# Optimization experiments

Measured on AMD Instinct MI355X. Metric: run time of the kernel, lower is better.

Reference implementation:

```python
import jax, jax.numpy as jnp
import numpy as np

EMBEDDING_DIM = 512
HEAD_DIM = 64
B, T_NEW, T_CACHE = 8, 1024, 3072
T_TOTAL = T_NEW + T_CACHE


def setup_inputs() -> dict:
    key = jax.random.key(0)
    ks = jax.random.split(key, 6)
    x = jax.random.normal(ks[0], (B, T_NEW, EMBEDDING_DIM), dtype=jnp.float32)
    cache_k = jax.random.normal(ks[1], (B, T_CACHE, HEAD_DIM), dtype=jnp.float32)
    cache_v = jax.random.normal(ks[2], (B, T_CACHE, HEAD_DIM), dtype=jnp.float32)
    # Causal mask rows for the new tokens: cache fully visible, causal among new.
    # Equivalent to tril(ones(T_TOTAL, T_TOTAL))[T_CACHE:, :].
    rows = jnp.arange(T_NEW)[:, None] + T_CACHE  # absolute positions of new tokens
    cols = jnp.arange(T_TOTAL)[None, :]
    mask = (cols <= rows).astype(jnp.int32)  # [T_NEW, T_TOTAL]
    scale = 1.0 / np.sqrt(EMBEDDING_DIM)
    Wq = jax.random.normal(ks[3], (EMBEDDING_DIM, HEAD_DIM), dtype=jnp.float32) * scale
    Wk = jax.random.normal(ks[4], (EMBEDDING_DIM, HEAD_DIM), dtype=jnp.float32) * scale
    Wv = jax.random.normal(ks[5], (EMBEDDING_DIM, HEAD_DIM), dtype=jnp.float32) * scale
    return {"x": x, "mask": mask, "cache_k": cache_k, "cache_v": cache_v,
            "Wq": Wq, "Wk": Wk, "Wv": Wv}


def reference(x, mask, cache_k, cache_v, Wq, Wk, Wv):
    # Projections (nn.Linear with bias=False)
    q = jnp.einsum("btc,cd->btd", x, Wq)  # [B, T_new, D]
    k_new = jnp.einsum("btc,cd->btd", x, Wk)
    v_new = jnp.einsum("btc,cd->btd", x, Wv)
    k = jnp.concatenate([cache_k, k_new], axis=1)  # [B, T_total, D]
    v = jnp.concatenate([cache_v, v_new], axis=1)
    d = k.shape[-1]
    scores = jnp.einsum("btd,bsd->bts", q, k) * (d ** -0.5)  # [B, T_new, T_total]
    T = q.shape[1]
    cur_mask = mask[:T, :k.shape[1]]  # [T_new, T_total]
    scores = jnp.where(cur_mask == 0, jnp.float32(-jnp.inf), scores)
    probs = jax.nn.softmax(scores, axis=-1)
    # Dropout is identity in eval mode (deterministic reference).
    out = jnp.einsum("bts,bsd->btd", probs, v)  # [B, T_new, D]
    return out, k, v
```

## Files before the change

kernel.cpp:

```cpp
#include <hip/hip_runtime.h>

#define NB     8
#define TNEW   1024
#define TCACHE 3072
#define TTOT   4096
#define EMB    512
#define HD     64

typedef __bf16 bf16x8 __attribute__((ext_vector_type(8)));
typedef __bf16 bf16x4 __attribute__((ext_vector_type(4)));
typedef float  f32x4  __attribute__((ext_vector_type(4)));

#define MFMA(a,b,c) __builtin_amdgcn_mfma_f32_16x16x32_bf16((a),(b),(c),0,0,0)

#define GLOAD_LDS16(g, l) \
    __builtin_amdgcn_global_load_lds((const __attribute__((address_space(1))) void*)(g), \
                                     (__attribute__((address_space(3))) void*)(l), 16, 0, 0)

#define QSCALE 0.180336880f

#define WS_WT   0
#define WS_KBF  196608
#define WS_VTB  4390912
#define WS_OP   8585216
#define WS_ML   16973824


__global__ __launch_bounds__(256) void prep(const float* __restrict__ ck,
                                            const float* __restrict__ cv,
                                            const float* __restrict__ Wq,
                                            const float* __restrict__ Wk,
                                            const float* __restrict__ Wv,
                                            float* __restrict__ kout,
                                            float* __restrict__ vout,
                                            __bf16* __restrict__ kb,
                                            __bf16* __restrict__ vtb,
                                            __bf16* __restrict__ wt) {
    __shared__ __bf16 vl[64][72];
    const int blk = blockIdx.x;
    const int tid = threadIdx.x;
    if (blk < 768) {
#pragma unroll
        for (int it = 0; it < 2; ++it) {
            const int i = blk * 256 + tid + it * 196608;
            const int b = i / 49152;
            const int f = i - b * 49152;
            const int s = f >> 4, d = (f & 15) * 4;
            const float4 kd = ((const float4*)ck)[i];
            ((float4*)(kout + (size_t)b * TTOT * HD))[f] = kd;
            bf16x4 k4;
            k4[0] = (__bf16)kd.x; k4[1] = (__bf16)kd.y;
            k4[2] = (__bf16)kd.z; k4[3] = (__bf16)kd.w;
            *(bf16x4*)(kb + (size_t)b * TTOT * HD + s * HD + d) = k4;
        }
    } else if (blk < 1152) {
        const int tb = blk - 768;
        const int b = tb / 48, si = tb - (tb / 48) * 48;
        const int sbase = si * 64;
        const float4* src = (const float4*)(cv + ((size_t)b * TCACHE + sbase) * HD);
        float4* dstf = (float4*)(vout + ((size_t)b * TTOT + sbase) * HD);
#pragma unroll
        for (int k = 0; k < 4; ++k) {
            const int f = tid + 256 * k;
            const int s = f >> 4, d4 = (f & 15) * 4;
            const float4 v = src[f];
            dstf[f] = v;
            bf16x4 t;
            t[0] = (__bf16)v.x; t[1] = (__bf16)v.y;
            t[2] = (__bf16)v.z; t[3] = (__bf16)v.w;
            *(bf16x4*)&vl[s][d4] = t;
        }
        __syncthreads();
        const int d = tid >> 2, sc = tid & 3;
        __bf16* vt = vtb + ((size_t)b * HD + d) * TTOT + sbase + (sc >> 1) * 32 + (sc & 1) * 4;
#pragma unroll
        for (int t4 = 0; t4 < 4; ++t4) {
            bf16x4 o;
#pragma unroll
            for (int c = 0; c < 4; ++c) o[c] = vl[sc * 16 + t4 * 4 + c][d];
            *(bf16x4*)(vt + t4 * 8) = o;
        }
    } else {
        const int tb = blk - 1152;
        const int m = tb >> 3;
        const int ct = (tb & 7) * 64;
        const float* W = (m == 0) ? Wq : (m == 1) ? Wk : Wv;
        const float4* src = (const float4*)(W + (size_t)ct * HD);
#pragma unroll
        for (int k = 0; k < 4; ++k) {
            const int f = tid + 256 * k;
            const int c = f >> 4, d4 = (f & 15) * 4;
            const float4 v = src[f];
            bf16x4 t;
            t[0] = (__bf16)v.x; t[1] = (__bf16)v.y;
            t[2] = (__bf16)v.z; t[3] = (__bf16)v.w;
            *(bf16x4*)&vl[c][d4] = t;
        }
        __syncthreads();
        const int d = tid >> 2, sc = tid & 3;
        bf16x8 o0, o1;
#pragma unroll
        for (int i = 0; i < 8; ++i) {
            o0[i] = vl[sc * 16 + i][d];
            o1[i] = vl[sc * 16 + 8 + i][d];
        }
        __bf16* wr = wt + (size_t)m * HD * EMB + (size_t)d * EMB + ct + sc * 16;
        *(bf16x8*)wr = o0;
        *(bf16x8*)(wr + 8) = o1;
    }
}

__global__ __launch_bounds__(128) void proj_mfma(const float* __restrict__ x,
                                                 const __bf16* __restrict__ wt,
                                                 __bf16* __restrict__ qb,
                                                 float* __restrict__ kout,
                                                 float* __restrict__ vout,
                                                 __bf16* __restrict__ kb,
                                                 __bf16* __restrict__ vtb) {
    __shared__ __bf16 xs[32][520];
    __shared__ __bf16 vls[2][64][24];
    const int tid = threadIdx.x;
    const int w = tid >> 6, lane = tid & 63;
    const int lo = lane & 15, hi = lane >> 4;
    const int r0 = blockIdx.x * 32 + w * 16;
    const int b = r0 >> 10;
    const int t0r = r0 & (TNEW - 1);

    {
        const float4* xg = (const float4*)(x + (size_t)blockIdx.x * 32 * EMB);
#pragma unroll
        for (int k = 0; k < 32; ++k) {
            const int f = tid + 128 * k;
            const int row = f >> 7, col4 = (f & 127) * 4;
            const float4 v = xg[f];
            bf16x4 t;
            t[0] = (__bf16)v.x; t[1] = (__bf16)v.y;
            t[2] = (__bf16)v.z; t[3] = (__bf16)v.w;
            *(bf16x4*)&xs[row][col4] = t;
        }
    }
    __syncthreads();

    for (int m = 0; m < 3; ++m) {
        const __bf16* wm = wt + (size_t)m * HD * EMB;
        f32x4 acc[4];
#pragma unroll
        for (int n = 0; n < 4; ++n) acc[n] = (f32x4){0.f, 0.f, 0.f, 0.f};
#pragma unroll
        for (int c = 0; c < 16; ++c) {
            const bf16x8 ax = *(const bf16x8*)&xs[w * 16 + lo][c * 32 + hi * 8];
#pragma unroll
            for (int n = 0; n < 4; ++n) {
                const bf16x8 bw = *(const bf16x8*)(wm + (size_t)(n * 16 + lo) * EMB + c * 32 + hi * 8);
                acc[n] = MFMA(ax, bw, acc[n]);
            }
        }
#pragma unroll
        for (int n = 0; n < 4; ++n) {
#pragma unroll
            for (int rr = 0; rr < 4; ++rr) {
                const int grow = r0 + hi * 4 + rr;
                const int t = grow & (TNEW - 1);
                const int d = n * 16 + lo;
                const float val = acc[n][rr];
                if (m == 0) {
                    qb[(size_t)grow * HD + d] = (__bf16)(val * QSCALE);
                } else if (m == 1) {
                    const size_t kv = ((size_t)b * TTOT + TCACHE + t) * HD + d;
                    kout[kv] = val;
                    kb[kv] = (__bf16)val;
                } else {
                    const size_t kv = ((size_t)b * TTOT + TCACHE + t) * HD + d;
                    vout[kv] = val;
                    vls[w][d][hi * 4 + rr] = (__bf16)val;
                }
            }
        }
    }
    __syncthreads();
    {
        const int tb4 = TCACHE + (t0r & ~63);
        const int m4 = (t0r >> 4) & 3;
        __bf16* vt = vtb + ((size_t)b * HD + lane) * TTOT + tb4 + (m4 >> 1) * 32 + (m4 & 1) * 4;
#pragma unroll
        for (int t4 = 0; t4 < 4; ++t4) {
            bf16x4 o;
#pragma unroll
            for (int c = 0; c < 4; ++c) o[c] = vls[w][lane][t4 * 4 + c];
            *(bf16x4*)(vt + t4 * 8) = o;
        }
    }
}

#define QB 128
#define NSPLIT 8
__global__ __launch_bounds__(512, 6) void attn_mfma(const __bf16* __restrict__ qb,
                                                    const __bf16* __restrict__ kb,
                                                    const __bf16* __restrict__ vtb,
                                                    __bf16* __restrict__ Opart,
                                                    float* __restrict__ mlpart) {
    __shared__ __align__(16) __bf16 Kt[3][64 * 64];
    __shared__ __align__(16) __bf16 Vts[3][64 * 64];

    const int tid = threadIdx.x;
    const int wv = tid >> 6, lane = tid & 63;
    const int lo = lane & 15, hi = lane >> 4;

    const int bid = blockIdx.x;
    const int b = bid & 7;
    const int idx = bid >> 3;
    const int split = idx & 7;
    const int qloc = idx >> 3;
    const int t0 = qloc * QB;
    const int row0 = b * TNEW + t0;

    const int ntiles = (TCACHE + t0 + QB) >> 6;
    const int count = (ntiles - split + 7) >> 3;

    const __bf16* Kb = kb + (size_t)b * TTOT * HD;
    const __bf16* Vb = vtb + (size_t)b * HD * TTOT;

    const int r_sub = lane >> 3;
    const int row_st = wv * 8 + r_sub;
    const int c_st = ((lane & 7) * 16) ^ (r_sub << 4);

#define STAGE(s, bi) do { \
        const char* gk_ = (const char*)Kb + (size_t)((s) + row_st) * 128 + c_st; \
        const char* gv_ = (const char*)Vb + ((size_t)row_st * TTOT + (s)) * 2 + c_st; \
        GLOAD_LDS16(gk_, Kt[bi] + row_st * 64); \
        GLOAD_LDS16(gv_, Vts[bi] + row_st * 64); \
    } while (0)

    const int t0w = t0 + wv * 16;
    const __bf16* Qw = qb + (size_t)(row0 + wv * 16) * HD;
    const bf16x8 aq0 = *(const bf16x8*)(Qw + (size_t)lo * HD + hi * 8);
    const bf16x8 aq1 = *(const bf16x8*)(Qw + (size_t)lo * HD + 32 + hi * 8);

    f32x4 o[4];
    float mg = -1e30f, lg = 0.f;
#pragma unroll
    for (int n = 0; n < 4; ++n) o[n] = (f32x4){0.f, 0.f, 0.f, 0.f};

    STAGE(split * 64, 0);
    if (count > 1) {
        STAGE(split * 64 + 512, 1);
        asm volatile("s_waitcnt vmcnt(2)" ::: "memory");
    } else {
        asm volatile("s_waitcnt vmcnt(0)" ::: "memory");
    }
    __builtin_amdgcn_s_barrier();
    __builtin_amdgcn_sched_barrier(0);

    const int sw = (lo & 7) << 3;

    int s0 = split * 64;
    int buf = 0;
    for (int it = 0; it < count; ++it, s0 += NSPLIT * 64) {
        const __bf16* Kl = Kt[buf];
        const __bf16* Vl = Vts[buf];

        const f32x4 z = (f32x4){0.f, 0.f, 0.f, 0.f};
        f32x4 sc[4];
#pragma unroll
        for (int kg = 0; kg < 4; ++kg) {
            const int kr = (kg * 16 + lo) * 64;
            const bf16x8 bk0 = *(const bf16x8*)(Kl + kr + ((hi * 8) ^ sw));
            const bf16x8 bk1 = *(const bf16x8*)(Kl + kr + ((32 + hi * 8) ^ sw));
            sc[kg] = MFMA(bk0, aq0, z);
            sc[kg] = MFMA(bk1, aq1, sc[kg]);
        }

        if (s0 + 63 > TCACHE + t0w) {
            const int lim = TCACHE + t0w + lo;
#pragma unroll
            for (int kg = 0; kg < 4; ++kg)
#pragma unroll
                for (int rr = 0; rr < 4; ++rr)
                    if (s0 + kg * 16 + hi * 4 + rr > lim) sc[kg][rr] = -1e30f;
        }

        f32x4 mx = sc[0];
        mx = (f32x4){fmaxf(mx[0], sc[1][0]), fmaxf(mx[1], sc[1][1]),
                     fmaxf(mx[2], sc[1][2]), fmaxf(mx[3], sc[1][3])};
        mx = (f32x4){fmaxf(mx[0], sc[2][0]), fmaxf(mx[1], sc[2][1]),
                     fmaxf(mx[2], sc[2][2]), fmaxf(mx[3], sc[2][3])};
        mx = (f32x4){fmaxf(mx[0], sc[3][0]), fmaxf(mx[1], sc[3][1]),
                     fmaxf(mx[2], sc[3][2]), fmaxf(mx[3], sc[3][3])};
        float mt = fmaxf(fmaxf(mx[0], mx[1]), fmaxf(mx[2], mx[3]));
        mt = fmaxf(mt, __shfl_xor(mt, 16));
        mt = fmaxf(mt, __shfl_xor(mt, 32));

        if (__any(mt > mg + 8.0f)) {
            const float mn = fmaxf(mg, mt);
            const float corr = exp2f(mg - mn);
            lg *= corr;
            mg = mn;
            float cb[4];
#pragma unroll
            for (int rr = 0; rr < 4; ++rr) cb[rr] = __shfl(corr, hi * 4 + rr);
#pragma unroll
            for (int n = 0; n < 4; ++n)
#pragma unroll
                for (int rr = 0; rr < 4; ++rr) o[n][rr] *= cb[rr];
        }

        float e[4][4];
        float ps = 0.f;
#pragma unroll
        for (int kg = 0; kg < 4; ++kg) {
#pragma unroll
            for (int rr = 0; rr < 4; ++rr) {
                e[kg][rr] = exp2f(sc[kg][rr] - mg);
                ps += e[kg][rr];
            }
        }
        ps += __shfl_xor(ps, 16);
        ps += __shfl_xor(ps, 32);
        lg += ps;

        bf16x8 ap0, ap1;
#pragma unroll
        for (int rr = 0; rr < 4; ++rr) {
            ap0[rr]     = (__bf16)e[0][rr];
            ap0[4 + rr] = (__bf16)e[1][rr];
            ap1[rr]     = (__bf16)e[2][rr];
            ap1[4 + rr] = (__bf16)e[3][rr];
        }

#pragma unroll
        for (int n = 0; n < 4; ++n) {
            const int vr = (n * 16 + lo) * 64;
            const bf16x8 bv0 = *(const bf16x8*)(Vl + vr + ((hi * 8) ^ sw));
            o[n] = MFMA(ap0, bv0, o[n]);
        }
#pragma unroll
        for (int n = 0; n < 4; ++n) {
            const int vr = (n * 16 + lo) * 64;
            const bf16x8 bv1 = *(const bf16x8*)(Vl + vr + ((32 + hi * 8) ^ sw));
            o[n] = MFMA(ap1, bv1, o[n]);
        }

        if (it + 2 < count) {
            int nb = buf + 2; if (nb >= 3) nb -= 3;
            STAGE(s0 + 2 * NSPLIT * 64, nb);
        }
        if (it + 1 < count) {
            if (it + 2 < count) { asm volatile("s_waitcnt vmcnt(2)" ::: "memory"); }
            else                { asm volatile("s_waitcnt vmcnt(0)" ::: "memory"); }
            __builtin_amdgcn_s_barrier();
            __builtin_amdgcn_sched_barrier(0);
        }
        buf = (buf == 2) ? 0 : buf + 1;
    }
#undef STAGE

    __bf16* Ow = Opart + ((size_t)split * (NB * TNEW) + row0 + wv * 16) * HD;
#pragma unroll
    for (int n = 0; n < 4; ++n)
#pragma unroll
        for (int rr = 0; rr < 4; ++rr)
            Ow[(size_t)(hi * 4 + rr) * HD + n * 16 + lo] = (__bf16)o[n][rr];
    if (hi == 0) {
        float* mlw = mlpart + ((size_t)split * (NB * TNEW) + row0 + wv * 16) * 2;
        mlw[lo * 2]     = mg;
        mlw[lo * 2 + 1] = lg;
    }
}

__global__ __launch_bounds__(256) void combine(const __bf16* __restrict__ Opart,
                                               const float* __restrict__ mlpart,
                                               float* __restrict__ out) {
    const int e = blockIdx.x * 256 + threadIdx.x;
    const int lane = threadIdx.x & 63;
    const int row = e >> 6, d = e & 63;
    const float2 ml2 = *(const float2*)&mlpart[(((size_t)(lane & 7)) * (NB * TNEW) + row) * 2];
    float mf = -1e30f;
#pragma unroll
    for (int s = 0; s < NSPLIT; ++s) mf = fmaxf(mf, __shfl(ml2.x, s));
    float lf = 0.f, acc = 0.f;
#pragma unroll
    for (int s = 0; s < NSPLIT; ++s) {
        const float ms = __shfl(ml2.x, s);
        const float ls = __shfl(ml2.y, s);
        const float f = exp2f(ms - mf);
        lf += ls * f;
        acc += (float)Opart[((size_t)s * (NB * TNEW) + row) * HD + d] * f;
    }
    out[e] = acc / lf;
}

extern "C" void kernel_launch(void* const* d_in, const int* in_sizes, int n_in,
                              void* d_out, int out_size, void* d_ws, size_t ws_size,
                              hipStream_t stream) {
    (void)in_sizes; (void)n_in; (void)out_size; (void)ws_size;
    const float* x  = (const float*)d_in[0];
    const float* ck = (const float*)d_in[2];
    const float* cv = (const float*)d_in[3];
    const float* Wq = (const float*)d_in[4];
    const float* Wk = (const float*)d_in[5];
    const float* Wv = (const float*)d_in[6];

    float* out  = (float*)d_out;
    float* kout = out + (size_t)NB * TNEW * HD;
    float* vout = kout + (size_t)NB * TTOT * HD;

    char* ws = (char*)d_ws;
    __bf16* wt  = (__bf16*)(ws + WS_WT);
    __bf16* kbf = (__bf16*)(ws + WS_KBF);
    __bf16* vtb = (__bf16*)(ws + WS_VTB);
    __bf16* Op  = (__bf16*)(ws + WS_OP);
    float*  ml  = (float*)(ws + WS_ML);
    __bf16* qb  = (__bf16*)d_out;

    prep<<<dim3(1176), dim3(256), 0, stream>>>(ck, cv, Wq, Wk, Wv, kout, vout, kbf, vtb, wt);
    proj_mfma<<<dim3(256), dim3(128), 0, stream>>>(x, wt, qb, kout, vout, kbf, vtb);
    attn_mfma<<<dim3(512), dim3(512), 0, stream>>>(qb, kbf, vtb, Op, ml);
    combine<<<dim3(2048), dim3(256), 0, stream>>>(Op, ml, out);
}
```

Measured before the change: 50.39 us.

## Give each attention wave two query groups and split projection by weight matrix

The attention kernel drops to 4 waves per block, and each wave handles two 16-row query groups. Each K/V tile loaded from LDS into registers is then reused across both groups, halving LDS reads per MFMA, at the cost of more registers and fewer waves to hide latency. Each wave now stages two rows per tile, so the waitcnt thresholds are adjusted to match. The projection kernel now uses 16-row blocks where waves 0-2 each compute one of Q/K/V in parallel, instead of looping over the three matrices serially. This doubles the number of blocks but leaves one wave per block idle.

New measurement: 53.75 us. 1.07x slower.

```diff
diff --git a/kernel.cpp b/kernel.cpp
--- a/kernel.cpp
+++ b/kernel.cpp
@@ -110,27 +110,27 @@
     }
 }
 
-__global__ __launch_bounds__(128) void proj_mfma(const float* __restrict__ x,
+__global__ __launch_bounds__(256) void proj_mfma(const float* __restrict__ x,
                                                  const __bf16* __restrict__ wt,
                                                  __bf16* __restrict__ qb,
                                                  float* __restrict__ kout,
                                                  float* __restrict__ vout,
                                                  __bf16* __restrict__ kb,
                                                  __bf16* __restrict__ vtb) {
-    __shared__ __bf16 xs[32][520];
-    __shared__ __bf16 vls[2][64][24];
+    __shared__ __bf16 xs[16][520];
+    __shared__ __bf16 vls[64][24];
     const int tid = threadIdx.x;
     const int w = tid >> 6, lane = tid & 63;
     const int lo = lane & 15, hi = lane >> 4;
-    const int r0 = blockIdx.x * 32 + w * 16;
+    const int r0 = blockIdx.x * 16;
     const int b = r0 >> 10;
     const int t0r = r0 & (TNEW - 1);
 
     {
-        const float4* xg = (const float4*)(x + (size_t)blockIdx.x * 32 * EMB);
-#pragma unroll
-        for (int k = 0; k < 32; ++k) {
-            const int f = tid + 128 * k;
+        const float4* xg = (const float4*)(x + (size_t)r0 * EMB);
+#pragma unroll
+        for (int k = 0; k < 8; ++k) {
+            const int f = tid + 256 * k;
             const int row = f >> 7, col4 = (f & 127) * 4;
             const float4 v = xg[f];
             bf16x4 t;
@@ -141,14 +141,15 @@
     }
     __syncthreads();
 
-    for (int m = 0; m < 3; ++m) {
+    if (w < 3) {
+        const int m = w;
         const __bf16* wm = wt + (size_t)m * HD * EMB;
         f32x4 acc[4];
 #pragma unroll
         for (int n = 0; n < 4; ++n) acc[n] = (f32x4){0.f, 0.f, 0.f, 0.f};
 #pragma unroll
         for (int c = 0; c < 16; ++c) {
-            const bf16x8 ax = *(const bf16x8*)&xs[w * 16 + lo][c * 32 + hi * 8];
+            const bf16x8 ax = *(const bf16x8*)&xs[lo][c * 32 + hi * 8];
 #pragma unroll
             for (int n = 0; n < 4; ++n) {
                 const bf16x8 bw = *(const bf16x8*)(wm + (size_t)(n * 16 + lo) * EMB + c * 32 + hi * 8);
@@ -172,29 +173,28 @@
                 } else {
                     const size_t kv = ((size_t)b * TTOT + TCACHE + t) * HD + d;
                     vout[kv] = val;
-                    vls[w][d][hi * 4 + rr] = (__bf16)val;
+                    vls[d][hi * 4 + rr] = (__bf16)val;
                 }
             }
         }
-    }
-    __syncthreads();
-    {
-        const int tb4 = TCACHE + (t0r & ~63);
-        const int m4 = (t0r >> 4) & 3;
-        __bf16* vt = vtb + ((size_t)b * HD + lane) * TTOT + tb4 + (m4 >> 1) * 32 + (m4 & 1) * 4;
-#pragma unroll
-        for (int t4 = 0; t4 < 4; ++t4) {
-            bf16x4 o;
-#pragma unroll
-            for (int c = 0; c < 4; ++c) o[c] = vls[w][lane][t4 * 4 + c];
-            *(bf16x4*)(vt + t4 * 8) = o;
+        if (m == 2) {
+            const int tb4 = TCACHE + (t0r & ~63);
+            const int m4 = (t0r >> 4) & 3;
+            __bf16* vt = vtb + ((size_t)b * HD + lane) * TTOT + tb4 + (m4 >> 1) * 32 + (m4 & 1) * 4;
+#pragma unroll
+            for (int t4 = 0; t4 < 4; ++t4) {
+                bf16x4 o;
+#pragma unroll
+                for (int c = 0; c < 4; ++c) o[c] = vls[lane][t4 * 4 + c];
+                *(bf16x4*)(vt + t4 * 8) = o;
+            }
         }
     }
 }
 
 #define QB 128
 #define NSPLIT 8
-__global__ __launch_bounds__(512, 6) void attn_mfma(const __bf16* __restrict__ qb,
+__global__ __launch_bounds__(256, 2) void attn_mfma(const __bf16* __restrict__ qb,
                                                     const __bf16* __restrict__ kb,
                                                     const __bf16* __restrict__ vtb,
                                                     __bf16* __restrict__ Opart,
@@ -221,30 +221,41 @@
     const __bf16* Vb = vtb + (size_t)b * HD * TTOT;
 
     const int r_sub = lane >> 3;
-    const int row_st = wv * 8 + r_sub;
     const int c_st = ((lane & 7) * 16) ^ (r_sub << 4);
 
 #define STAGE(s, bi) do { \
-        const char* gk_ = (const char*)Kb + (size_t)((s) + row_st) * 128 + c_st; \
-        const char* gv_ = (const char*)Vb + ((size_t)row_st * TTOT + (s)) * 2 + c_st; \
-        GLOAD_LDS16(gk_, Kt[bi] + row_st * 64); \
-        GLOAD_LDS16(gv_, Vts[bi] + row_st * 64); \
+        _Pragma("unroll") \
+        for (int j_ = 0; j_ < 2; ++j_) { \
+            const int row_ = wv * 16 + j_ * 8 + r_sub; \
+            const char* gk_ = (const char*)Kb + (size_t)((s) + row_) * 128 + c_st; \
+            const char* gv_ = (const char*)Vb + ((size_t)row_ * TTOT + (s)) * 2 + c_st; \
+            GLOAD_LDS16(gk_, Kt[bi] + row_ * 64); \
+            GLOAD_LDS16(gv_, Vts[bi] + row_ * 64); \
+        } \
     } while (0)
 
-    const int t0w = t0 + wv * 16;
-    const __bf16* Qw = qb + (size_t)(row0 + wv * 16) * HD;
-    const bf16x8 aq0 = *(const bf16x8*)(Qw + (size_t)lo * HD + hi * 8);
-    const bf16x8 aq1 = *(const bf16x8*)(Qw + (size_t)lo * HD + 32 + hi * 8);
-
-    f32x4 o[4];
-    float mg = -1e30f, lg = 0.f;
-#pragma unroll
-    for (int n = 0; n < 4; ++n) o[n] = (f32x4){0.f, 0.f, 0.f, 0.f};
+    const int t0w = t0 + wv * 32;
+    const __bf16* Qw = qb + (size_t)(row0 + wv * 32) * HD;
+    bf16x8 aq[2][2];
+#pragma unroll
+    for (int g = 0; g < 2; ++g) {
+        aq[g][0] = *(const bf16x8*)(Qw + (size_t)(g * 16 + lo) * HD + hi * 8);
+        aq[g][1] = *(const bf16x8*)(Qw + (size_t)(g * 16 + lo) * HD + 32 + hi * 8);
+    }
+
+    f32x4 o[2][4];
+    float mg[2], lg[2];
+#pragma unroll
+    for (int g = 0; g < 2; ++g) {
+#pragma unroll
+        for (int n = 0; n < 4; ++n) o[g][n] = (f32x4){0.f, 0.f, 0.f, 0.f};
+        mg[g] = -1e30f; lg[g] = 0.f;
+    }
 
     STAGE(split * 64, 0);
     if (count > 1) {
         STAGE(split * 64 + 512, 1);
-        asm volatile("s_waitcnt vmcnt(2)" ::: "memory");
+        asm volatile("s_waitcnt vmcnt(4)" ::: "memory");
     } else {
         asm volatile("s_waitcnt vmcnt(0)" ::: "memory");
     }
@@ -259,85 +270,92 @@
         const __bf16* Kl = Kt[buf];
         const __bf16* Vl = Vts[buf];
 
-        const f32x4 z = (f32x4){0.f, 0.f, 0.f, 0.f};
-        f32x4 sc[4];
+        bf16x8 bk[4][2], bv[4][2];
 #pragma unroll
         for (int kg = 0; kg < 4; ++kg) {
             const int kr = (kg * 16 + lo) * 64;
-            const bf16x8 bk0 = *(const bf16x8*)(Kl + kr + ((hi * 8) ^ sw));
-            const bf16x8 bk1 = *(const bf16x8*)(Kl + kr + ((32 + hi * 8) ^ sw));
-            sc[kg] = MFMA(bk0, aq0, z);
-            sc[kg] = MFMA(bk1, aq1, sc[kg]);
-        }
-
-        if (s0 + 63 > TCACHE + t0w) {
-            const int lim = TCACHE + t0w + lo;
-#pragma unroll
-            for (int kg = 0; kg < 4; ++kg)
-#pragma unroll
-                for (int rr = 0; rr < 4; ++rr)
-                    if (s0 + kg * 16 + hi * 4 + rr > lim) sc[kg][rr] = -1e30f;
-        }
-
-        f32x4 mx = sc[0];
-        mx = (f32x4){fmaxf(mx[0], sc[1][0]), fmaxf(mx[1], sc[1][1]),
-                     fmaxf(mx[2], sc[1][2]), fmaxf(mx[3], sc[1][3])};
-        mx = (f32x4){fmaxf(mx[0], sc[2][0]), fmaxf(mx[1], sc[2][1]),
-                     fmaxf(mx[2], sc[2][2]), fmaxf(mx[3], sc[2][3])};
-        mx = (f32x4){fmaxf(mx[0], sc[3][0]), fmaxf(mx[1], sc[3][1]),
-                     fmaxf(mx[2], sc[3][2]), fmaxf(mx[3], sc[3][3])};
-        float mt = fmaxf(fmaxf(mx[0], mx[1]), fmaxf(mx[2], mx[3]));
-        mt = fmaxf(mt, __shfl_xor(mt, 16));
-        mt = fmaxf(mt, __shfl_xor(mt, 32));
-
-        if (__any(mt > mg + 8.0f)) {
-            const float mn = fmaxf(mg, mt);
-            const float corr = exp2f(mg - mn);
-            lg *= corr;
-            mg = mn;
-            float cb[4];
-#pragma unroll
-            for (int rr = 0; rr < 4; ++rr) cb[rr] = __shfl(corr, hi * 4 + rr);
-#pragma unroll
-            for (int n = 0; n < 4; ++n)
-#pragma unroll
-                for (int rr = 0; rr < 4; ++rr) o[n][rr] *= cb[rr];
-        }
-
-        float e[4][4];
-        float ps = 0.f;
-#pragma unroll
-        for (int kg = 0; kg < 4; ++kg) {
-#pragma unroll
-            for (int rr = 0; rr < 4; ++rr) {
-                e[kg][rr] = exp2f(sc[kg][rr] - mg);
-                ps += e[kg][rr];
-            }
-        }
-        ps += __shfl_xor(ps, 16);
-        ps += __shfl_xor(ps, 32);
-        lg += ps;
-
-        bf16x8 ap0, ap1;
-#pragma unroll
-        for (int rr = 0; rr < 4; ++rr) {
-            ap0[rr]     = (__bf16)e[0][rr];
-            ap0[4 + rr] = (__bf16)e[1][rr];
-            ap1[rr]     = (__bf16)e[2][rr];
-            ap1[4 + rr] = (__bf16)e[3][rr];
-        }
-
+            bk[kg][0] = *(const bf16x8*)(Kl + kr + ((hi * 8) ^ sw));
+            bk[kg][1] = *(const bf16x8*)(Kl + kr + ((32 + hi * 8) ^ sw));
+        }
 #pragma unroll
         for (int n = 0; n < 4; ++n) {
             const int vr = (n * 16 + lo) * 64;
-            const bf16x8 bv0 = *(const bf16x8*)(Vl + vr + ((hi * 8) ^ sw));
-            o[n] = MFMA(ap0, bv0, o[n]);
-        }
-#pragma unroll
-        for (int n = 0; n < 4; ++n) {
-            const int vr = (n * 16 + lo) * 64;
-            const bf16x8 bv1 = *(const bf16x8*)(Vl + vr + ((32 + hi * 8) ^ sw));
-            o[n] = MFMA(ap1, bv1, o[n]);
+            bv[n][0] = *(const bf16x8*)(Vl + vr + ((hi * 8) ^ sw));
+            bv[n][1] = *(const bf16x8*)(Vl + vr + ((32 + hi * 8) ^ sw));
+        }
+
+#pragma unroll
+        for (int g = 0; g < 2; ++g) {
+            const int tg = t0w + g * 16;
+            const f32x4 z = (f32x4){0.f, 0.f, 0.f, 0.f};
+            f32x4 sc[4];
+#pragma unroll
+            for (int kg = 0; kg < 4; ++kg) {
+                sc[kg] = MFMA(bk[kg][0], aq[g][0], z);
+                sc[kg] = MFMA(bk[kg][1], aq[g][1], sc[kg]);
+            }
+
+            if (s0 + 63 > TCACHE + tg) {
+                const int lim = TCACHE + tg + lo;
+#pragma unroll
+                for (int kg = 0; kg < 4; ++kg)
+#pragma unroll
+                    for (int rr = 0; rr < 4; ++rr)
+                        if (s0 + kg * 16 + hi * 4 + rr > lim) sc[kg][rr] = -1e30f;
+            }
+
+            f32x4 mx = sc[0];
+            mx = (f32x4){fmaxf(mx[0], sc[1][0]), fmaxf(mx[1], sc[1][1]),
+                         fmaxf(mx[2], sc[1][2]), fmaxf(mx[3], sc[1][3])};
+            mx = (f32x4){fmaxf(mx[0], sc[2][0]), fmaxf(mx[1], sc[2][1]),
+                         fmaxf(mx[2], sc[2][2]), fmaxf(mx[3], sc[2][3])};
+            mx = (f32x4){fmaxf(mx[0], sc[3][0]), fmaxf(mx[1], sc[3][1]),
+                         fmaxf(mx[2], sc[3][2]), fmaxf(mx[3], sc[3][3])};
+            float mt = fmaxf(fmaxf(mx[0], mx[1]), fmaxf(mx[2], mx[3]));
+            mt = fmaxf(mt, __shfl_xor(mt, 16));
+            mt = fmaxf(mt, __shfl_xor(mt, 32));
+
+            if (__any(mt > mg[g] + 8.0f)) {
+                const float mn = fmaxf(mg[g], mt);
+                const float corr = exp2f(mg[g] - mn);
+                lg[g] *= corr;
+                mg[g] = mn;
+                float cb[4];
+#pragma unroll
+                for (int rr = 0; rr < 4; ++rr) cb[rr] = __shfl(corr, hi * 4 + rr);
+#pragma unroll
+                for (int n = 0; n < 4; ++n)
+#pragma unroll
+                    for (int rr = 0; rr < 4; ++rr) o[g][n][rr] *= cb[rr];
+            }
+
+            float e[4][4];
+            float ps = 0.f;
+#pragma unroll
+            for (int kg = 0; kg < 4; ++kg) {
+#pragma unroll
+                for (int rr = 0; rr < 4; ++rr) {
+                    e[kg][rr] = exp2f(sc[kg][rr] - mg[g]);
+                    ps += e[kg][rr];
+                }
+            }
+            ps += __shfl_xor(ps, 16);
+            ps += __shfl_xor(ps, 32);
+            lg[g] += ps;
+
+            bf16x8 ap0, ap1;
+#pragma unroll
+            for (int rr = 0; rr < 4; ++rr) {
+                ap0[rr]     = (__bf16)e[0][rr];
+                ap0[4 + rr] = (__bf16)e[1][rr];
+                ap1[rr]     = (__bf16)e[2][rr];
+                ap1[4 + rr] = (__bf16)e[3][rr];
+            }
+
+#pragma unroll
+            for (int n = 0; n < 4; ++n) o[g][n] = MFMA(ap0, bv[n][0], o[g][n]);
+#pragma unroll
+            for (int n = 0; n < 4; ++n) o[g][n] = MFMA(ap1, bv[n][1], o[g][n]);
         }
 
         if (it + 2 < count) {
@@ -345,7 +363,7 @@
             STAGE(s0 + 2 * NSPLIT * 64, nb);
         }
         if (it + 1 < count) {
-            if (it + 2 < count) { asm volatile("s_waitcnt vmcnt(2)" ::: "memory"); }
+            if (it + 2 < count) { asm volatile("s_waitcnt vmcnt(4)" ::: "memory"); }
             else                { asm volatile("s_waitcnt vmcnt(0)" ::: "memory"); }
             __builtin_amdgcn_s_barrier();
             __builtin_amdgcn_sched_barrier(0);
@@ -354,16 +372,19 @@
     }
 #undef STAGE
 
-    __bf16* Ow = Opart + ((size_t)split * (NB * TNEW) + row0 + wv * 16) * HD;
-#pragma unroll
-    for (int n = 0; n < 4; ++n)
-#pragma unroll
-        for (int rr = 0; rr < 4; ++rr)
-            Ow[(size_t)(hi * 4 + rr) * HD + n * 16 + lo] = (__bf16)o[n][rr];
-    if (hi == 0) {
-        float* mlw = mlpart + ((size_t)split * (NB * TNEW) + row0 + wv * 16) * 2;
-        mlw[lo * 2]     = mg;
-        mlw[lo * 2 + 1] = lg;
+#pragma unroll
+    for (int g = 0; g < 2; ++g) {
+        __bf16* Ow = Opart + ((size_t)split * (NB * TNEW) + row0 + wv * 32 + g * 16) * HD;
+#pragma unroll
+        for (int n = 0; n < 4; ++n)
+#pragma unroll
+            for (int rr = 0; rr < 4; ++rr)
+                Ow[(size_t)(hi * 4 + rr) * HD + n * 16 + lo] = (__bf16)o[g][n][rr];
+        if (hi == 0) {
+            float* mlw = mlpart + ((size_t)split * (NB * TNEW) + row0 + wv * 32 + g * 16) * 2;
+            mlw[lo * 2]     = mg[g];
+            mlw[lo * 2 + 1] = lg[g];
+        }
     }
 }
 
@@ -413,7 +434,7 @@
     __bf16* qb  = (__bf16*)d_out;
 
     prep<<<dim3(1176), dim3(256), 0, stream>>>(ck, cv, Wq, Wk, Wv, kout, vout, kbf, vtb, wt);
-    proj_mfma<<<dim3(256), dim3(128), 0, stream>>>(x, wt, qb, kout, vout, kbf, vtb);
-    attn_mfma<<<dim3(512), dim3(512), 0, stream>>>(qb, kbf, vtb, Op, ml);
+    proj_mfma<<<dim3(512), dim3(256), 0, stream>>>(x, wt, qb, kout, vout, kbf, vtb);
+    attn_mfma<<<dim3(512), dim3(256), 0, stream>>>(qb, kbf, vtb, Op, ml);
     combine<<<dim3(2048), dim3(256), 0, stream>>>(Op, ml, out);
 }
```

## Split weight prep into tiny kernel, merge projection with cache conversion

Applied to the files above, without the earlier changes.

Moves the weight transpose/convert into a small separate kernel and merges the x-projection with the K/V cache copy and conversion into one launch. Each projection block now handles 16 rows, with one wave per Q/K/V matrix, so the three projections run in parallel instead of looping. The aim is for the cache-copy blocks to overlap with the projection MFMA work and for the larger block count to fill the GPU better. In exchange, the fourth wave of each projection block sits idle, and x rows are loaded once per 16 rows instead of once per 32.

Measured after the change: 51.94 us. 3.1% more time.

```diff
diff --git a/kernel.cpp b/kernel.cpp
--- a/kernel.cpp
+++ b/kernel.cpp
@@ -26,23 +26,132 @@
 #define WS_ML   16973824
 
 
-__global__ __launch_bounds__(256) void prep(const float* __restrict__ ck,
+__global__ __launch_bounds__(256) void wprep(const float* __restrict__ Wq,
+                                             const float* __restrict__ Wk,
+                                             const float* __restrict__ Wv,
+                                             __bf16* __restrict__ wt) {
+    __shared__ __bf16 vl[64][72];
+    const int tid = threadIdx.x;
+    const int tb = blockIdx.x;
+    const int m = tb >> 3;
+    const int ct = (tb & 7) * 64;
+    const float* W = (m == 0) ? Wq : (m == 1) ? Wk : Wv;
+    const float4* src = (const float4*)(W + (size_t)ct * HD);
+#pragma unroll
+    for (int k = 0; k < 4; ++k) {
+        const int f = tid + 256 * k;
+        const int c = f >> 4, d4 = (f & 15) * 4;
+        const float4 v = src[f];
+        bf16x4 t;
+        t[0] = (__bf16)v.x; t[1] = (__bf16)v.y;
+        t[2] = (__bf16)v.z; t[3] = (__bf16)v.w;
+        *(bf16x4*)&vl[c][d4] = t;
+    }
+    __syncthreads();
+    const int d = tid >> 2, sc = tid & 3;
+    bf16x8 o0, o1;
+#pragma unroll
+    for (int i = 0; i < 8; ++i) {
+        o0[i] = vl[sc * 16 + i][d];
+        o1[i] = vl[sc * 16 + 8 + i][d];
+    }
+    __bf16* wr = wt + (size_t)m * HD * EMB + (size_t)d * EMB + ct + sc * 16;
+    *(bf16x8*)wr = o0;
+    *(bf16x8*)(wr + 8) = o1;
+}
+
+#define SM_BYTES 19712
+__global__ __launch_bounds__(256) void work(const float* __restrict__ x,
+                                            const float* __restrict__ ck,
                                             const float* __restrict__ cv,
-                                            const float* __restrict__ Wq,
-                                            const float* __restrict__ Wk,
-                                            const float* __restrict__ Wv,
+                                            const __bf16* __restrict__ wt,
                                             float* __restrict__ kout,
                                             float* __restrict__ vout,
                                             __bf16* __restrict__ kb,
                                             __bf16* __restrict__ vtb,
-                                            __bf16* __restrict__ wt) {
-    __shared__ __bf16 vl[64][72];
+                                            __bf16* __restrict__ qb) {
+    __shared__ __align__(16) char smem[SM_BYTES];
     const int blk = blockIdx.x;
     const int tid = threadIdx.x;
-    if (blk < 768) {
+
+    if (blk < 512) {
+        __bf16 (*xs)[520] = (__bf16(*)[520])smem;
+        __bf16 (*vls)[24] = (__bf16(*)[24])(smem + 16640);
+        const int w = tid >> 6, lane = tid & 63;
+        const int lo = lane & 15, hi = lane >> 4;
+        const int r0 = blk * 16;
+        const int b = r0 >> 10;
+        const int t0r = r0 & (TNEW - 1);
+
+        {
+            const float4* xg = (const float4*)(x + (size_t)r0 * EMB);
+#pragma unroll
+            for (int k = 0; k < 8; ++k) {
+                const int f = tid + 256 * k;
+                const int row = f >> 7, col4 = (f & 127) * 4;
+                const float4 v = xg[f];
+                bf16x4 t;
+                t[0] = (__bf16)v.x; t[1] = (__bf16)v.y;
+                t[2] = (__bf16)v.z; t[3] = (__bf16)v.w;
+                *(bf16x4*)&xs[row][col4] = t;
+            }
+        }
+        __syncthreads();
+
+        if (w < 3) {
+            const int m = w;
+            const __bf16* wm = wt + (size_t)m * HD * EMB;
+            f32x4 acc[4];
+#pragma unroll
+            for (int n = 0; n < 4; ++n) acc[n] = (f32x4){0.f, 0.f, 0.f, 0.f};
+#pragma unroll
+            for (int c = 0; c < 16; ++c) {
+                const bf16x8 ax = *(const bf16x8*)&xs[lo][c * 32 + hi * 8];
+#pragma unroll
+                for (int n = 0; n < 4; ++n) {
+                    const bf16x8 bw = *(const bf16x8*)(wm + (size_t)(n * 16 + lo) * EMB + c * 32 + hi * 8);
+                    acc[n] = MFMA(ax, bw, acc[n]);
+                }
+            }
+#pragma unroll
+            for (int n = 0; n < 4; ++n) {
+#pragma unroll
+                for (int rr = 0; rr < 4; ++rr) {
+                    const int grow = r0 + hi * 4 + rr;
+                    const int t = grow & (TNEW - 1);
+                    const int d = n * 16 + lo;
+                    const float val = acc[n][rr];
+                    if (m == 0) {
+                        qb[(size_t)grow * HD + d] = (__bf16)(val * QSCALE);
+                    } else if (m == 1) {
+                        const size_t kv = ((size_t)b * TTOT + TCACHE + t) * HD + d;
+                        kout[kv] = val;
+                        kb[kv] = (__bf16)val;
+                    } else {
+                        const size_t kv = ((size_t)b * TTOT + TCACHE + t) * HD + d;
+                        vout[kv] = val;
+                        vls[d][hi * 4 + rr] = (__bf16)val;
+                    }
+                }
+            }
+            if (m == 2) {
+                const int tb4 = TCACHE + (t0r & ~63);
+                const int m4 = (t0r >> 4) & 3;
+                __bf16* vt = vtb + ((size_t)b * HD + lane) * TTOT + tb4 + (m4 >> 1) * 32 + (m4 & 1) * 4;
+#pragma unroll
+                for (int t4 = 0; t4 < 4; ++t4) {
+                    bf16x4 o;
+#pragma unroll
+                    for (int c = 0; c < 4; ++c) o[c] = vls[lane][t4 * 4 + c];
+                    *(bf16x4*)(vt + t4 * 8) = o;
+                }
+            }
+        }
+    } else if (blk < 1280) {
+        const int kblk = blk - 512;
 #pragma unroll
         for (int it = 0; it < 2; ++it) {
-            const int i = blk * 256 + tid + it * 196608;
+            const int i = kblk * 256 + tid + it * 196608;
             const int b = i / 49152;
             const int f = i - b * 49152;
             const int s = f >> 4, d = (f & 15) * 4;
@@ -53,8 +162,9 @@
             k4[2] = (__bf16)kd.z; k4[3] = (__bf16)kd.w;
             *(bf16x4*)(kb + (size_t)b * TTOT * HD + s * HD + d) = k4;
         }
-    } else if (blk < 1152) {
-        const int tb = blk - 768;
+    } else {
+        __bf16 (*vl)[72] = (__bf16(*)[72])smem;
+        const int tb = blk - 1280;
         const int b = tb / 48, si = tb - (tb / 48) * 48;
         const int sbase = si * 64;
         const float4* src = (const float4*)(cv + ((size_t)b * TCACHE + sbase) * HD);
@@ -78,115 +188,6 @@
             bf16x4 o;
 #pragma unroll
             for (int c = 0; c < 4; ++c) o[c] = vl[sc * 16 + t4 * 4 + c][d];
-            *(bf16x4*)(vt + t4 * 8) = o;
-        }
-    } else {
-        const int tb = blk - 1152;
-        const int m = tb >> 3;
-        const int ct = (tb & 7) * 64;
-        const float* W = (m == 0) ? Wq : (m == 1) ? Wk : Wv;
-        const float4* src = (const float4*)(W + (size_t)ct * HD);
-#pragma unroll
-        for (int k = 0; k < 4; ++k) {
-            const int f = tid + 256 * k;
-            const int c = f >> 4, d4 = (f & 15) * 4;
-            const float4 v = src[f];
-            bf16x4 t;
-            t[0] = (__bf16)v.x; t[1] = (__bf16)v.y;
-            t[2] = (__bf16)v.z; t[3] = (__bf16)v.w;
-            *(bf16x4*)&vl[c][d4] = t;
-        }
-        __syncthreads();
-        const int d = tid >> 2, sc = tid & 3;
-        bf16x8 o0, o1;
-#pragma unroll
-        for (int i = 0; i < 8; ++i) {
-            o0[i] = vl[sc * 16 + i][d];
-            o1[i] = vl[sc * 16 + 8 + i][d];
-        }
-        __bf16* wr = wt + (size_t)m * HD * EMB + (size_t)d * EMB + ct + sc * 16;
-        *(bf16x8*)wr = o0;
-        *(bf16x8*)(wr + 8) = o1;
-    }
-}
-
-__global__ __launch_bounds__(128) void proj_mfma(const float* __restrict__ x,
-                                                 const __bf16* __restrict__ wt,
-                                                 __bf16* __restrict__ qb,
-                                                 float* __restrict__ kout,
-                                                 float* __restrict__ vout,
-                                                 __bf16* __restrict__ kb,
-                                                 __bf16* __restrict__ vtb) {
-    __shared__ __bf16 xs[32][520];
-    __shared__ __bf16 vls[2][64][24];
-    const int tid = threadIdx.x;
-    const int w = tid >> 6, lane = tid & 63;
-    const int lo = lane & 15, hi = lane >> 4;
-    const int r0 = blockIdx.x * 32 + w * 16;
-    const int b = r0 >> 10;
-    const int t0r = r0 & (TNEW - 1);
-
-    {
-        const float4* xg = (const float4*)(x + (size_t)blockIdx.x * 32 * EMB);
-#pragma unroll
-        for (int k = 0; k < 32; ++k) {
-            const int f = tid + 128 * k;
-            const int row = f >> 7, col4 = (f & 127) * 4;
-            const float4 v = xg[f];
-            bf16x4 t;
-            t[0] = (__bf16)v.x; t[1] = (__bf16)v.y;
-            t[2] = (__bf16)v.z; t[3] = (__bf16)v.w;
-            *(bf16x4*)&xs[row][col4] = t;
-        }
-    }
-    __syncthreads();
-
-    for (int m = 0; m < 3; ++m) {
-        const __bf16* wm = wt + (size_t)m * HD * EMB;
-        f32x4 acc[4];
-#pragma unroll
-        for (int n = 0; n < 4; ++n) acc[n] = (f32x4){0.f, 0.f, 0.f, 0.f};
-#pragma unroll
-        for (int c = 0; c < 16; ++c) {
-            const bf16x8 ax = *(const bf16x8*)&xs[w * 16 + lo][c * 32 + hi * 8];
-#pragma unroll
-            for (int n = 0; n < 4; ++n) {
-                const bf16x8 bw = *(const bf16x8*)(wm + (size_t)(n * 16 + lo) * EMB + c * 32 + hi * 8);
-                acc[n] = MFMA(ax, bw, acc[n]);
-            }
-        }
-#pragma unroll
-        for (int n = 0; n < 4; ++n) {
-#pragma unroll
-            for (int rr = 0; rr < 4; ++rr) {
-                const int grow = r0 + hi * 4 + rr;
-                const int t = grow & (TNEW - 1);
-                const int d = n * 16 + lo;
-                const float val = acc[n][rr];
-                if (m == 0) {
-                    qb[(size_t)grow * HD + d] = (__bf16)(val * QSCALE);
-                } else if (m == 1) {
-                    const size_t kv = ((size_t)b * TTOT + TCACHE + t) * HD + d;
-                    kout[kv] = val;
-                    kb[kv] = (__bf16)val;
-                } else {
-                    const size_t kv = ((size_t)b * TTOT + TCACHE + t) * HD + d;
-                    vout[kv] = val;
-                    vls[w][d][hi * 4 + rr] = (__bf16)val;
-                }
-            }
-        }
-    }
-    __syncthreads();
-    {
-        const int tb4 = TCACHE + (t0r & ~63);
-        const int m4 = (t0r >> 4) & 3;
-        __bf16* vt = vtb + ((size_t)b * HD + lane) * TTOT + tb4 + (m4 >> 1) * 32 + (m4 & 1) * 4;
-#pragma unroll
-        for (int t4 = 0; t4 < 4; ++t4) {
-            bf16x4 o;
-#pragma unroll
-            for (int c = 0; c < 4; ++c) o[c] = vls[w][lane][t4 * 4 + c];
             *(bf16x4*)(vt + t4 * 8) = o;
         }
     }
@@ -412,8 +413,8 @@
     float*  ml  = (float*)(ws + WS_ML);
     __bf16* qb  = (__bf16*)d_out;
 
-    prep<<<dim3(1176), dim3(256), 0, stream>>>(ck, cv, Wq, Wk, Wv, kout, vout, kbf, vtb, wt);
-    proj_mfma<<<dim3(256), dim3(128), 0, stream>>>(x, wt, qb, kout, vout, kbf, vtb);
+    wprep<<<dim3(24), dim3(256), 0, stream>>>(Wq, Wk, Wv, wt);
+    work<<<dim3(1664), dim3(256), 0, stream>>>(x, ck, cv, wt, kout, vout, kbf, vtb, qb);
     attn_mfma<<<dim3(512), dim3(512), 0, stream>>>(qb, kbf, vtb, Op, ml);
     combine<<<dim3(2048), dim3(256), 0, stream>>>(Op, ml, out);
 }
```

## Fuse split-K combine into attention kernel via last-block atomic counter

Applied to the files above, without the earlier changes.

Removes the separate combine kernel. Each attention block increments a per-(batch, query-block) counter after writing its partial O and m/l values, and the last of the eight split blocks merges them into the final output. The counters are zeroed in the prep kernel. This saves one kernel launch and lets the reduction overlap with other attention blocks, at the cost of fences and atomics plus a serial tail in the last block. The launch-bounds occupancy hint also drops from 6 to 4. There is a risk: the output region aliases the bf16 Q buffer, so writing early could clobber Q rows that blocks still running have not yet read.

Result: slower. 188.0 us (+273.1%).

```diff
diff --git a/kernel.cpp b/kernel.cpp
--- a/kernel.cpp
+++ b/kernel.cpp
@@ -24,6 +24,7 @@
 #define WS_VTB  4390912
 #define WS_OP   8585216
 #define WS_ML   16973824
+#define WS_CNT  17498112
 
 
 __global__ __launch_bounds__(256) void prep(const float* __restrict__ ck,
@@ -35,10 +36,12 @@
                                             float* __restrict__ vout,
                                             __bf16* __restrict__ kb,
                                             __bf16* __restrict__ vtb,
-                                            __bf16* __restrict__ wt) {
+                                            __bf16* __restrict__ wt,
+                                            int* __restrict__ cnt) {
     __shared__ __bf16 vl[64][72];
     const int blk = blockIdx.x;
     const int tid = threadIdx.x;
+    if (blk == 1152 && tid < 64) cnt[tid] = 0;
     if (blk < 768) {
 #pragma unroll
         for (int it = 0; it < 2; ++it) {
@@ -194,13 +197,16 @@
 
 #define QB 128
 #define NSPLIT 8
-__global__ __launch_bounds__(512, 6) void attn_mfma(const __bf16* __restrict__ qb,
+__global__ __launch_bounds__(512, 4) void attn_mfma(const __bf16* __restrict__ qb,
                                                     const __bf16* __restrict__ kb,
                                                     const __bf16* __restrict__ vtb,
                                                     __bf16* __restrict__ Opart,
-                                                    float* __restrict__ mlpart) {
+                                                    float* __restrict__ mlpart,
+                                                    float* __restrict__ out,
+                                                    int* __restrict__ cnt) {
     __shared__ __align__(16) __bf16 Kt[3][64 * 64];
     __shared__ __align__(16) __bf16 Vts[3][64 * 64];
+    __shared__ int sflag;
 
     const int tid = threadIdx.x;
     const int wv = tid >> 6, lane = tid & 63;
@@ -365,28 +371,34 @@
         mlw[lo * 2]     = mg;
         mlw[lo * 2 + 1] = lg;
     }
-}
-
-__global__ __launch_bounds__(256) void combine(const __bf16* __restrict__ Opart,
-                                               const float* __restrict__ mlpart,
-                                               float* __restrict__ out) {
-    const int e = blockIdx.x * 256 + threadIdx.x;
-    const int lane = threadIdx.x & 63;
-    const int row = e >> 6, d = e & 63;
-    const float2 ml2 = *(const float2*)&mlpart[(((size_t)(lane & 7)) * (NB * TNEW) + row) * 2];
-    float mf = -1e30f;
-#pragma unroll
-    for (int s = 0; s < NSPLIT; ++s) mf = fmaxf(mf, __shfl(ml2.x, s));
-    float lf = 0.f, acc = 0.f;
-#pragma unroll
-    for (int s = 0; s < NSPLIT; ++s) {
-        const float ms = __shfl(ml2.x, s);
-        const float ls = __shfl(ml2.y, s);
-        const float f = exp2f(ms - mf);
-        lf += ls * f;
-        acc += (float)Opart[((size_t)s * (NB * TNEW) + row) * HD + d] * f;
-    }
-    out[e] = acc / lf;
+
+    __threadfence();
+    __syncthreads();
+    if (tid == 0) sflag = atomicAdd(&cnt[b * 8 + qloc], 1);
+    __syncthreads();
+    if (sflag == NSPLIT - 1) {
+        __threadfence();
+        for (int ee = tid; ee < QB * HD; ee += 512) {
+            const int r = ee >> 6, d = ee & 63;
+            const int row = row0 + r;
+            float ms[NSPLIT], ls[NSPLIT];
+            float mf = -1e30f;
+#pragma unroll
+            for (int s = 0; s < NSPLIT; ++s) {
+                const float2 v2 = *(const float2*)&mlpart[((size_t)s * (NB * TNEW) + row) * 2];
+                ms[s] = v2.x; ls[s] = v2.y;
+                mf = fmaxf(mf, v2.x);
+            }
+            float lf = 0.f, acc = 0.f;
+#pragma unroll
+            for (int s = 0; s < NSPLIT; ++s) {
+                const float f = exp2f(ms[s] - mf);
+                lf += ls[s] * f;
+                acc += (float)Opart[((size_t)s * (NB * TNEW) + row) * HD + d] * f;
+            }
+            out[(size_t)row * HD + d] = acc / lf;
+        }
+    }
 }
 
 extern "C" void kernel_launch(void* const* d_in, const int* in_sizes, int n_in,
@@ -410,10 +422,10 @@
     __bf16* vtb = (__bf16*)(ws + WS_VTB);
     __bf16* Op  = (__bf16*)(ws + WS_OP);
     float*  ml  = (float*)(ws + WS_ML);
+    int*    cnt = (int*)(ws + WS_CNT);
     __bf16* qb  = (__bf16*)d_out;
 
-    prep<<<dim3(1176), dim3(256), 0, stream>>>(ck, cv, Wq, Wk, Wv, kout, vout, kbf, vtb, wt);
+    prep<<<dim3(1176), dim3(256), 0, stream>>>(ck, cv, Wq, Wk, Wv, kout, vout, kbf, vtb, wt, cnt);
     proj_mfma<<<dim3(256), dim3(128), 0, stream>>>(x, wt, qb, kout, vout, kbf, vtb);
-    attn_mfma<<<dim3(512), dim3(512), 0, stream>>>(qb, kbf, vtb, Op, ml);
-    combine<<<dim3(2048), dim3(256), 0, stream>>>(Op, ml, out);
+    attn_mfma<<<dim3(512), dim3(512), 0, stream>>>(qb, kbf, vtb, Op, ml, out, cnt);
 }
```
